# Performance work log

Hardware: AMD Instinct MI355X
Metric: run time of the kernel (lower is better)

Reference implementation:

```python
import jax, jax.numpy as jnp
import numpy as np

DT = 0.02
GRAVITY = jnp.array([0.0, -9.81, 0.0], dtype=jnp.float32)
RADIUS = 0.1125  # filter_extent/2 = 6*radius_scale*particle_radius/2
K3 = 4
TAPS = K3 ** 3
EPS = 1e-8
N_FLUID, N_BOX, KNBR = 8192, 4096, 48
BOX_L = 1.12
CORNERS = np.array([[dx, dy, dz] for dx in (0, 1) for dy in (0, 1) for dz in (0, 1)], np.int32)  # [8,3]


def _ball_to_cube(p):
    """Volume-preserving map unit-ball -> unit-cube (ball->cylinder->cube), per Open3D CConv."""
    x, y, z = p[..., 0], p[..., 1], p[..., 2]
    rxy2 = x * x + y * y
    rho = jnp.sqrt(rxy2 + z * z + EPS)
    rxy = jnp.sqrt(rxy2 + EPS)
    # ball -> cylinder
    pole = rxy2 <= 1.25 * z * z
    s_pole = jnp.sqrt(3.0 * rho / (rho + jnp.abs(z)))
    s_side = rho / rxy
    cx = jnp.where(pole, x * s_pole, x * s_side)
    cy = jnp.where(pole, y * s_pole, y * s_side)
    cz = jnp.where(pole, jnp.sign(z) * rho, 1.5 * z)
    # cylinder disc -> square (inverse concentric map)
    r = jnp.sqrt(cx * cx + cy * cy + EPS)
    cond = jnp.abs(cx) >= jnp.abs(cy)
    sx = jnp.where(cx >= 0, 1.0, -1.0)
    sy = jnp.where(cy >= 0, 1.0, -1.0)
    safe_cx = jnp.where(jnp.abs(cx) > EPS, cx, 1.0)
    safe_cy = jnp.where(jnp.abs(cy) > EPS, cy, 1.0)
    c4pi = 4.0 / jnp.pi
    u = jnp.where(cond, sx * r, sy * c4pi * r * jnp.arctan(cx / safe_cy))
    v = jnp.where(cond, sx * c4pi * r * jnp.arctan(cy / safe_cx), sy * r)
    tiny = rho < 1e-6
    return jnp.stack([jnp.where(tiny, 0.0, u), jnp.where(tiny, 0.0, v), jnp.where(tiny, 0.0, cz)], axis=-1)


def _cconv(feat_in, pos_in, pos_out, nbr_idx, filt, bias):
    """ContinuousConv: radius neighbors (padded, -1), poly6 window, trilinear interp over 4^3 taps."""
    Nq, K = nbr_idx.shape
    mask = (nbr_idx >= 0).astype(feat_in.dtype)
    idx = jnp.maximum(nbr_idx, 0)
    rel = (pos_in[idx] - pos_out[:, None, :]) / RADIUS            # [Nq,K,3]
    d2 = jnp.sum(rel * rel, axis=-1)
    win = jnp.clip((1.0 - d2) ** 3, 0.0, 1.0) * mask              # poly6 window on r^2
    cube = _ball_to_cube(rel)                                     # [-1,1]^3
    t = jnp.clip((cube * 0.5 + 0.5) * (K3 - 1), 0.0, K3 - 1.0)    # align_corners grid coords
    i0 = jnp.clip(jnp.floor(t), 0, K3 - 2).astype(jnp.int32)
    f = t - i0
    ci = i0[..., None, :] + CORNERS                               # [Nq,K,8,3]
    cw = jnp.prod(jnp.where(CORNERS[None, None] == 1, f[..., None, :], 1.0 - f[..., None, :]), axis=-1)
    tap = (ci[..., 0] * K3 + ci[..., 1]) * K3 + ci[..., 2]        # [Nq,K,8]
    cw = cw * win[..., None]
    ii = jnp.arange(Nq)[:, None, None]
    kk = jnp.arange(K)[None, :, None]
    Wt = jnp.zeros((Nq, K, TAPS), feat_in.dtype).at[ii, kk, tap].add(cw)  # [Nq,K,64]
    fnb = feat_in[idx]                                            # [Nq,K,Cin]
    A = jnp.einsum('nkt,nkc->ntc', Wt, fnb)                       # per-tap aggregated features
    return jnp.einsum('ntc,tcd->nd', A, filt.reshape(TAPS, filt.shape[-2], filt.shape[-1])) + bias


def _forward(pos, vel, box, box_feats, nbr_fluid, nbr_box, params):
    (cf0_w, cf0_b, co0_w, co0_b, d0_w, d0_b,
     c1_w, c1_b, d1_w, d1_b, c2_w, c2_b, d2_w, d2_b, c3_w, c3_b, d3_w, d3_b) = params
    vel_new = vel + GRAVITY * DT
    pos_new = pos + (vel + vel_new) * (0.5 * DT)
    fluid_feats = jnp.concatenate([jnp.ones_like(pos_new[:, :1]), vel_new], axis=-1)  # [N,4]
    a_conv = _cconv(fluid_feats, pos_new, pos_new, nbr_fluid, cf0_w, cf0_b)
    a_dense = fluid_feats @ d0_w + d0_b
    a_obs = _cconv(box_feats, box, pos_new, nbr_box, co0_w, co0_b)
    x = jnp.concatenate([a_obs, a_conv, a_dense], axis=-1)        # [N,96]
    for cw_, cb_, dw_, db_ in ((c1_w, c1_b, d1_w, d1_b), (c2_w, c2_b, d2_w, d2_b), (c3_w, c3_b, d3_w, d3_b)):
        h = jax.nn.relu(x)
        y = _cconv(h, pos_new, pos_new, nbr_fluid, cw_, cb_) + (h @ dw_ + db_)
        x = y + x if y.shape[-1] == x.shape[-1] else y            # dense residual when dims match
    pos_correction = x * (1.0 / 128.0)
    pos_new_corrected = pos_new + pos_correction
    vel_new_corrected = (pos_new_corrected - pos) / DT
    num_fluid_neighbors = jnp.sum((nbr_fluid >= 0).astype(jnp.float32), axis=-1)
    return pos_new_corrected, vel_new_corrected, num_fluid_neighbors


def _build_neighbors(queries, points, radius, K, exclude_self):
    N = queries.shape[0]
    idx = np.full((N, K), -1, np.int32)
    r2 = radius * radius
    chunk = 1024
    for s in range(0, N, chunk):
        q = queries[s:s + chunk]
        d2 = ((q[:, None, :] - points[None, :, :]) ** 2).sum(-1)
        within = d2 <= r2
        if exclude_self:
            rows = np.arange(q.shape[0])
            within[rows, s + rows] = False
        for r in range(q.shape[0]):
            nb = np.nonzero(within[r])[0][:K]
            idx[s + r, :nb.shape[0]] = nb
    return idx


def setup_inputs() -> dict:
    rng = np.random.default_rng(0)
    pos = rng.uniform(0.0, BOX_L, (N_FLUID, 3)).astype(np.float32)
    vel = (0.5 * rng.standard_normal((N_FLUID, 3))).astype(np.float32)
    box = rng.uniform(0.0, BOX_L, (N_BOX, 3)).astype(np.float32)
    box_feats = rng.standard_normal((N_BOX, 3)).astype(np.float32)
    g = np.array([0.0, -9.81, 0.0], np.float32)
    vel_new = vel + g * DT
    pos_new = pos + (vel + vel_new) * (0.5 * DT)
    nbr_fluid = _build_neighbors(pos_new, pos_new, RADIUS, KNBR, True)
    nbr_box = _build_neighbors(pos_new, box, RADIUS, KNBR, False)

    def xavier(*shape):
        fan_in = int(np.prod(shape[:-1]))
        lim = float(np.sqrt(6.0 / (fan_in + shape[-1])))
        return jnp.asarray(rng.uniform(-lim, lim, shape).astype(np.float32))

    z = lambda n: jnp.zeros((n,), jnp.float32)
    return {
        'pos': jnp.asarray(pos), 'vel': jnp.asarray(vel), 'box': jnp.asarray(box),
        'box_feats': jnp.asarray(box_feats),
        'nbr_fluid': jnp.asarray(nbr_fluid), 'nbr_box': jnp.asarray(nbr_box),
        'cf0_w': xavier(4, 4, 4, 4, 32), 'cf0_b': z(32),
        'co0_w': xavier(4, 4, 4, 3, 32), 'co0_b': z(32),
        'd0_w': xavier(4, 32), 'd0_b': z(32),
        'c1_w': xavier(4, 4, 4, 96, 64), 'c1_b': z(64), 'd1_w': xavier(96, 64), 'd1_b': z(64),
        'c2_w': xavier(4, 4, 4, 64, 64), 'c2_b': z(64), 'd2_w': xavier(64, 64), 'd2_b': z(64),
        'c3_w': xavier(4, 4, 4, 64, 3), 'c3_b': z(3), 'd3_w': xavier(64, 3), 'd3_b': z(3),
    }


def reference(pos, vel, box, box_feats, nbr_fluid, nbr_box,
              cf0_w, cf0_b, co0_w, co0_b, d0_w, d0_b,
              c1_w, c1_b, d1_w, d1_b, c2_w, c2_b, d2_w, d2_b, c3_w, c3_b, d3_w, d3_b):
    params = (cf0_w, cf0_b, co0_w, co0_b, d0_w, d0_b,
              c1_w, c1_b, d1_w, d1_b, c2_w, c2_b, d2_w, d2_b, c3_w, c3_b, d3_w, d3_b)
    return _forward(pos, vel, box, box_feats, nbr_fluid, nbr_box, params)
```

## Files before the change

kernel.cpp:

```cpp
#include <hip/hip_runtime.h>

#define NF 8192
#define KN 48
#define TM 8

typedef __attribute__((ext_vector_type(8))) short short8;
typedef __attribute__((ext_vector_type(4))) float f32x4;

__device__ __forceinline__ unsigned short bf16e(float f) {
    return (unsigned short)((__float_as_uint(f) + 0x8000u) >> 16);
}

__device__ __forceinline__ void pn_geom(float rx, float ry, float rz, unsigned* g)
{
    float d2  = rx * rx + ry * ry + rz * rz;
    float om  = 1.0f - d2;
    float win = om * om * om;
    win = fminf(fmaxf(win, 0.0f), 1.0f);

    float rxy2 = rx * rx + ry * ry;
    float rho  = sqrtf(rxy2 + rz * rz + 1e-8f);
    float rxyv = sqrtf(rxy2 + 1e-8f);
    bool  pole = (rxy2 <= 1.25f * rz * rz);
    float s    = pole ? sqrtf(3.0f * rho / (rho + fabsf(rz))) : (rho / rxyv);
    float cx = rx * s, cy = ry * s;
    float sgnz = (rz > 0.0f) ? 1.0f : ((rz < 0.0f) ? -1.0f : 0.0f);
    float cz   = pole ? sgnz * rho : 1.5f * rz;

    float rr   = sqrtf(cx * cx + cy * cy + 1e-8f);
    bool  cond = fabsf(cx) >= fabsf(cy);
    float sx = (cx >= 0.0f) ? 1.0f : -1.0f;
    float sy = (cy >= 0.0f) ? 1.0f : -1.0f;
    float safecx = (fabsf(cx) > 1e-8f) ? cx : 1.0f;
    float safecy = (fabsf(cy) > 1e-8f) ? cy : 1.0f;
    const float C4PI = 1.2732395447351628f;
    float u = cond ? (sx * rr) : (sy * C4PI * rr * atanf(cx / safecy));
    float v = cond ? (sx * C4PI * rr * atanf(cy / safecx)) : (sy * rr);
    if (rho < 1e-6f) { u = 0.0f; v = 0.0f; cz = 0.0f; }

    float tx = fminf(fmaxf((u  * 0.5f + 0.5f) * 3.0f, 0.0f), 3.0f);
    float ty = fminf(fmaxf((v  * 0.5f + 0.5f) * 3.0f, 0.0f), 3.0f);
    float tz = fminf(fmaxf((cz * 0.5f + 0.5f) * 3.0f, 0.0f), 3.0f);
    int ix = (int)floorf(tx); ix = ix < 0 ? 0 : (ix > 2 ? 2 : ix);
    int iy = (int)floorf(ty); iy = iy < 0 ? 0 : (iy > 2 ? 2 : iy);
    int iz = (int)floorf(tz); iz = iz < 0 ? 0 : (iz > 2 ? 2 : iz);
    float fx = tx - (float)ix, fy = ty - (float)iy, fz = tz - (float)iz;
    float wx0 = 1.0f - fx, wy0 = 1.0f - fy, wz0 = 1.0f - fz;

#pragma unroll
    for (int dx = 0; dx < 2; ++dx)
#pragma unroll
        for (int dy = 0; dy < 2; ++dy)
#pragma unroll
            for (int dz = 0; dz < 2; ++dz) {
                float w = (dx ? fx : wx0) * (dy ? fy : wy0) * (dz ? fz : wz0) * win;
                int tap = ((ix + dx) << 4) + ((iy + dy) << 2) + (iz + dz);
                g[(dx << 2) | (dy << 1) | dz] = ((unsigned)tap << 16) | (unsigned)bf16e(w);
            }
}

__global__ void __launch_bounds__(256) pn_prep(
    const float* __restrict__ pos, const float* __restrict__ vel,
    const int* __restrict__ nbrf,
    const float* __restrict__ d0w, const float* __restrict__ d0b,
    float* __restrict__ pos_new, float* __restrict__ feats0,
    float* __restrict__ X, float* __restrict__ nfn)
{
    int t = blockIdx.x * 256 + threadIdx.x;
    if (t >= NF) return;
    float vx = vel[t * 3 + 0], vy = vel[t * 3 + 1], vz = vel[t * 3 + 2];
    float vnx = vx, vny = vy - 9.81f * 0.02f, vnz = vz;
    float pnx = pos[t * 3 + 0] + (vx + vnx) * 0.01f;
    float pny = pos[t * 3 + 1] + (vy + vny) * 0.01f;
    float pnz = pos[t * 3 + 2] + (vz + vnz) * 0.01f;
    pos_new[t * 3 + 0] = pnx; pos_new[t * 3 + 1] = pny; pos_new[t * 3 + 2] = pnz;
    feats0[t * 4 + 0] = 1.0f; feats0[t * 4 + 1] = vnx;
    feats0[t * 4 + 2] = vny;  feats0[t * 4 + 3] = vnz;
    int cnt = 0;
    for (int k = 0; k < KN; ++k) cnt += (nbrf[t * KN + k] >= 0) ? 1 : 0;
    nfn[t] = (float)cnt;
    for (int j = 0; j < 32; ++j) {
        float s = d0b[j] + d0w[0 * 32 + j] + vnx * d0w[1 * 32 + j]
                + vny * d0w[2 * 32 + j] + vnz * d0w[3 * 32 + j];
        X[t * 96 + 64 + j] = s;
    }
}

template <int CIN, int COUT, int HAS_SELF>
__global__ void __launch_bounds__(256) pn_pack(
    const float* __restrict__ cw, const float* __restrict__ dw,
    const float* __restrict__ cb, const float* __restrict__ db,
    unsigned short* __restrict__ F2t, unsigned short* __restrict__ FD,
    float* __restrict__ B)
{
    constexpr int CINP = ((CIN + 15) / 16) * 16;
    constexpr int NCC  = CINP / 16;
    constexpr int DPAD = ((COUT + 15) / 16) * 16;
    constexpr int NT   = DPAD / 16;
    const int total1 = NCC * NT * 16 * 1024;
    const int total2 = HAS_SELF ? DPAD * CINP : 0;
    int i = blockIdx.x * 256 + threadIdx.x;
    if (i < total1) {
        int k2 = i & 1023;
        int q  = i >> 10;
        int dd = q & 15; q >>= 4;
        int dt = q % NT;
        int cc = q / NT;
        int t   = k2 >> 4;
        int cin = cc * 16 + (k2 & 15);
        int d   = dt * 16 + dd;
        float v = 0.0f;
        if (cin < CIN && d < COUT) v = cw[((size_t)t * CIN + cin) * COUT + d];
        F2t[i] = bf16e(v);
    } else if (i < total1 + total2) {
        int j = i - total1;
        int d = j / CINP, c = j % CINP;
        float v = 0.0f;
        if (c < CIN && d < COUT) v = dw[(size_t)c * COUT + d];
        FD[j] = bf16e(v);
    }
    if (i < COUT) B[i] = cb[i] + (HAS_SELF ? db[i] : 0.0f);
}

template <int CIN, int COUT, int HAS_SELF, int RELU_IN, int OUT_MODE>
__global__ void __launch_bounds__(512, 4) pn_cconv(
    const float* __restrict__ qpos, const float* __restrict__ ppos,
    const float* __restrict__ feats, const int* __restrict__ nbr,
    const unsigned short* __restrict__ F2t, const unsigned short* __restrict__ FD,
    const float* __restrict__ bias,
    const float* __restrict__ resid, float* __restrict__ outp,
    const float* __restrict__ pos0, int out_stride, int out_off)
{
    constexpr int CINP   = ((CIN + 15) / 16) * 16;
    constexpr int NCC    = CINP / 16;
    constexpr int DPAD   = ((COUT + 15) / 16) * 16;
    constexpr int NT     = DPAD / 16;
    constexpr int SPLITK = 8 / NT;
    constexpr int SPC2   = 32 / SPLITK;
    constexpr int WST    = 48;
    constexpr int A2ST   = 1032;

    __shared__ int      sI[TM * KN];
    __shared__ int      sKN[TM];
    __shared__ __align__(16) unsigned short sW [TM * 64 * WST];
    __shared__ __align__(16) unsigned short sFT[TM * 16 * WST];
    __shared__ __align__(16) unsigned short sA2[TM * A2ST];

    float*          sEpi = (float*)sFT;
    unsigned short* sA3  = sFT + 4096;

    const int tid  = threadIdx.x;
    const int w    = tid >> 6;
    const int lane = tid & 63;
    const int n16  = lane & 15;
    const int kg   = lane >> 4;
    const int pt0  = blockIdx.x * TM;
    const int dt   = w % NT;
    const int kh   = w / NT;

    if (tid < TM) sKN[tid] = KN;
    {
        uint4 z4 = make_uint4(0, 0, 0, 0);
        for (int i = tid; i < TM * 64 * WST / 8; i += 512) ((uint4*)sW)[i] = z4;
    }
    __syncthreads();

    for (int e = tid; e < TM * KN; e += 512) {
        int lp = e / KN, k = e - lp * KN;
        int q  = pt0 + lp;
        int id = nbr[q * KN + k];
        if (id >= 0) {
            sI[e] = id;
            float rx = (ppos[id * 3 + 0] - qpos[q * 3 + 0]) * (1.0f / 0.1125f);
            float ry = (ppos[id * 3 + 1] - qpos[q * 3 + 1]) * (1.0f / 0.1125f);
            float rz = (ppos[id * 3 + 2] - qpos[q * 3 + 2]) * (1.0f / 0.1125f);
            unsigned g[8];
            pn_geom(rx, ry, rz, g);
#pragma unroll
            for (int j = 0; j < 8; ++j)
                sW[(lp * 64 + (int)(g[j] >> 16)) * WST + k] = (unsigned short)(g[j] & 0xffffu);
        } else {
            atomicMin(&sKN[lp], k);
        }
    }

    f32x4 acc = {0.0f, 0.0f, 0.0f, 0.0f};
    __syncthreads();

    for (int cc = 0; cc < NCC; ++cc) {
        const int cb0 = cc * 16;

        for (int e = tid; e < TM * KN; e += 512) {
            int pt = e / KN, k = e - pt * KN;
            unsigned short vals[16];
            if (k < sKN[pt]) {
                int id = sI[e];
                if constexpr (CIN % 16 == 0) {
                    const float4* s4 = (const float4*)(feats + (size_t)id * CIN + cb0);
#pragma unroll
                    for (int v4 = 0; v4 < 4; ++v4) {
                        float4 f = s4[v4];
                        if (RELU_IN) { f.x=fmaxf(f.x,0.f); f.y=fmaxf(f.y,0.f); f.z=fmaxf(f.z,0.f); f.w=fmaxf(f.w,0.f); }
                        vals[v4*4+0] = bf16e(f.x); vals[v4*4+1] = bf16e(f.y);
                        vals[v4*4+2] = bf16e(f.z); vals[v4*4+3] = bf16e(f.w);
                    }
                } else {
#pragma unroll
                    for (int c = 0; c < 16; ++c) {
                        float f = (cb0 + c < CIN) ? feats[(size_t)id * CIN + cb0 + c] : 0.0f;
                        if (RELU_IN) f = fmaxf(f, 0.0f);
                        vals[c] = bf16e(f);
                    }
                }
            } else {
#pragma unroll
                for (int c = 0; c < 16; ++c) vals[c] = 0;
            }
#pragma unroll
            for (int c = 0; c < 16; ++c) sFT[(pt * 16 + c) * WST + k] = vals[c];
        }
        __syncthreads();

        {
            const short8 z8 = {0,0,0,0,0,0,0,0};
            short8 bv[2];
#pragma unroll
            for (int s = 0; s < 2; ++s) {
                int kidx = s * 32 + kg * 8;
                bv[s] = z8;
                if (kidx < KN)
                    bv[s] = *(const short8*)(sFT + (w * 16 + n16) * WST + kidx);
            }
#pragma unroll
            for (int mt = 0; mt < 4; ++mt) {
                f32x4 a1 = {0.0f, 0.0f, 0.0f, 0.0f};
#pragma unroll
                for (int s = 0; s < 2; ++s) {
                    int kidx = s * 32 + kg * 8;
                    short8 av = z8;
                    if (kidx < KN)
                        av = *(const short8*)(sW + (w * 64 + mt * 16 + n16) * WST + kidx);
                    a1 = __builtin_amdgcn_mfma_f32_16x16x32_bf16(av, bv[s], a1, 0, 0, 0);
                }
#pragma unroll
                for (int r = 0; r < 4; ++r)
                    sA2[w * A2ST + (mt * 16 + kg * 4 + r) * 16 + n16] = bf16e(a1[r]);
            }
        }
        __syncthreads();

        {
            const unsigned short* gB = F2t + ((size_t)((cc * NT + dt) * 16 + n16)) * 1024;
            const int s0 = kh * SPC2;
            const short8 z8 = {0,0,0,0,0,0,0,0};
#pragma unroll 4
            for (int s2 = 0; s2 < SPC2; ++s2) {
                int k2 = (s0 + s2) * 32 + kg * 8;
                short8 av = (n16 < TM) ? *(const short8*)(sA2 + n16 * A2ST + k2) : z8;
                short8 bv = *(const short8*)(gB + k2);
                acc = __builtin_amdgcn_mfma_f32_16x16x32_bf16(av, bv, acc, 0, 0, 0);
            }
        }
        __syncthreads();
    }

    if constexpr (HAS_SELF) {
        constexpr int NP = NCC / 2;
        for (int ccp = 0; ccp < NP; ++ccp) {
            if (tid < TM * 32) {
                int pt = tid / 32, c = tid & 31;
                int cin = ccp * 32 + c;
                float f = (cin < CIN) ? feats[(size_t)(pt0 + pt) * CIN + cin] : 0.0f;
                if (RELU_IN) f = fmaxf(f, 0.0f);
                sA3[pt * 40 + c] = bf16e(f);
            }
            __syncthreads();
            if (ccp % SPLITK == kh) {
                const short8 z8 = {0,0,0,0,0,0,0,0};
                short8 av = (n16 < TM) ? *(const short8*)(sA3 + n16 * 40 + kg * 8) : z8;
                short8 bv = *(const short8*)(FD + (size_t)(dt * 16 + n16) * CINP + ccp * 32 + kg * 8);
                acc = __builtin_amdgcn_mfma_f32_16x16x32_bf16(av, bv, acc, 0, 0, 0);
            }
            __syncthreads();
        }
    }

#pragma unroll
    for (int r = 0; r < 4; ++r) sEpi[(w * 64 + lane) * 4 + r] = acc[r];
    __syncthreads();

    if (w < NT) {
        float sum[4];
#pragma unroll
        for (int r = 0; r < 4; ++r) {
            float s = 0.0f;
#pragma unroll
            for (int k = 0; k < SPLITK; ++k)
                s += sEpi[((k * NT + w) * 64 + lane) * 4 + r];
            sum[r] = s;
        }
        int d = w * 16 + n16;
        if (d < COUT) {
            float b = bias[d];
#pragma unroll
            for (int r = 0; r < 4; ++r) {
                int pt = kg * 4 + r;
                if (pt < TM) {
                    int q = pt0 + pt;
                    float y = sum[r] + b;
                    if constexpr (OUT_MODE == 0) {
                        outp[q * out_stride + out_off + d] = y;
                    } else if constexpr (OUT_MODE == 1) {
                        outp[q * COUT + d] = y;
                    } else if constexpr (OUT_MODE == 2) {
                        outp[q * COUT + d] = y + resid[q * COUT + d];
                    } else {
                        float corr = y * (1.0f / 128.0f);
                        float pn   = qpos[q * 3 + d];
                        float pc   = pn + corr;
                        outp[q * 3 + d]          = pc;
                        outp[NF * 3 + q * 3 + d] = (pc - pos0[q * 3 + d]) * (1.0f / 0.02f);
                    }
                }
            }
        }
    }
}

extern "C" void kernel_launch(void* const* d_in, const int* in_sizes, int n_in,
                              void* d_out, int out_size, void* d_ws, size_t ws_size,
                              hipStream_t stream)
{
    (void)in_sizes; (void)n_in; (void)out_size; (void)ws_size;

    const float* pos       = (const float*)d_in[0];
    const float* vel       = (const float*)d_in[1];
    const float* box       = (const float*)d_in[2];
    const float* box_feats = (const float*)d_in[3];
    const int*   nbrf      = (const int*)d_in[4];
    const int*   nbrb      = (const int*)d_in[5];
    const float* cf0_w = (const float*)d_in[6];
    const float* cf0_b = (const float*)d_in[7];
    const float* co0_w = (const float*)d_in[8];
    const float* co0_b = (const float*)d_in[9];
    const float* d0_w  = (const float*)d_in[10];
    const float* d0_b  = (const float*)d_in[11];
    const float* c1_w  = (const float*)d_in[12];
    const float* c1_b  = (const float*)d_in[13];
    const float* d1_w  = (const float*)d_in[14];
    const float* d1_b  = (const float*)d_in[15];
    const float* c2_w  = (const float*)d_in[16];
    const float* c2_b  = (const float*)d_in[17];
    const float* d2_w  = (const float*)d_in[18];
    const float* d2_b  = (const float*)d_in[19];
    const float* c3_w  = (const float*)d_in[20];
    const float* c3_b  = (const float*)d_in[21];
    const float* d3_w  = (const float*)d_in[22];
    const float* d3_b  = (const float*)d_in[23];

    char* ws = (char*)d_ws;
    float*          POSNEW = (float*)(ws + 0);
    float*          FEATS0 = (float*)(ws + 98304);
    float*          X      = (float*)(ws + 229376);
    float*          X1     = (float*)(ws + 3375104);
    float*          X2     = (float*)(ws + 5472256);
    unsigned short* F2T1   = (unsigned short*)(ws + 7569408);
    unsigned short* F2T2   = (unsigned short*)(ws + 8355840);
    unsigned short* F2T3   = (unsigned short*)(ws + 8880128);
    unsigned short* F2Tf   = (unsigned short*)(ws + 9011200);
    unsigned short* F2To   = (unsigned short*)(ws + 9076736);
    unsigned short* FD1    = (unsigned short*)(ws + 9142272);
    unsigned short* FD2    = (unsigned short*)(ws + 9154560);
    unsigned short* FD3    = (unsigned short*)(ws + 9162752);
    float*          B1     = (float*)(ws + 9164800);
    float*          B2     = (float*)(ws + 9165056);
    float*          B3     = (float*)(ws + 9165312);
    float*          Bf0    = (float*)(ws + 9165568);
    float*          Bo0    = (float*)(ws + 9165824);

    float* out_f = (float*)d_out;

    pn_pack<96, 64, 1><<<(6*4*16*1024 + 64*96 + 255) / 256, 256, 0, stream>>>(c1_w, d1_w, c1_b, d1_b, F2T1, FD1, B1);
    pn_pack<64, 64, 1><<<(4*4*16*1024 + 64*64 + 255) / 256, 256, 0, stream>>>(c2_w, d2_w, c2_b, d2_b, F2T2, FD2, B2);
    pn_pack<64, 3, 1><<<(4*1*16*1024 + 16*64 + 255) / 256, 256, 0, stream>>>(c3_w, d3_w, c3_b, d3_b, F2T3, FD3, B3);
    pn_pack<4, 32, 0><<<(1*2*16*1024 + 255) / 256, 256, 0, stream>>>(cf0_w, nullptr, cf0_b, nullptr, F2Tf, nullptr, Bf0);
    pn_pack<3, 32, 0><<<(1*2*16*1024 + 255) / 256, 256, 0, stream>>>(co0_w, nullptr, co0_b, nullptr, F2To, nullptr, Bo0);

    pn_prep<<<(NF + 255) / 256, 256, 0, stream>>>(pos, vel, nbrf, d0_w, d0_b,
                                                  POSNEW, FEATS0, X, out_f + NF * 6);

    pn_cconv<4, 32, 0, 0, 0><<<NF / TM, 512, 0, stream>>>(
        POSNEW, POSNEW, FEATS0, nbrf, F2Tf, nullptr, Bf0, nullptr, X, nullptr, 96, 32);
    pn_cconv<3, 32, 0, 0, 0><<<NF / TM, 512, 0, stream>>>(
        POSNEW, box, box_feats, nbrb, F2To, nullptr, Bo0, nullptr, X, nullptr, 96, 0);
    pn_cconv<96, 64, 1, 1, 1><<<NF / TM, 512, 0, stream>>>(
        POSNEW, POSNEW, X, nbrf, F2T1, FD1, B1, nullptr, X1, nullptr, 0, 0);
    pn_cconv<64, 64, 1, 1, 2><<<NF / TM, 512, 0, stream>>>(
        POSNEW, POSNEW, X1, nbrf, F2T2, FD2, B2, X1, X2, nullptr, 0, 0);
    pn_cconv<64, 3, 1, 1, 3><<<NF / TM, 512, 0, stream>>>(
        POSNEW, POSNEW, X2, nbrf, F2T3, FD3, B3, nullptr, out_f, pos, 0, 0);
}
```

Before: 369.2 us.

## Halve tap-weight LDS via two tap-half passes and pipeline feature staging

Splits the 64-tap interpolation weights into two passes of 32 taps, halving the sW and sA2 shared buffers, and raises launch bounds so more blocks fit per CU. Neighbor geometry is now kept in registers, one thread per neighbor, which removes the sI/sKN arrays and the atomicMin. Staging of the next channel chunk is moved between the two MFMA stages to overlap global loads with compute, and two accumulators break the MFMA dependency chain. The cost is recomputing sW scatters and re-staging features for each half, plus extra register pressure under the tighter launch bound.

```diff
diff --git a/kernel.cpp b/kernel.cpp
--- a/kernel.cpp
+++ b/kernel.cpp
@@ -123,7 +123,7 @@
 }
 
 template <int CIN, int COUT, int HAS_SELF, int RELU_IN, int OUT_MODE>
-__global__ void __launch_bounds__(512, 4) pn_cconv(
+__global__ void __launch_bounds__(512, 6) pn_cconv(
     const float* __restrict__ qpos, const float* __restrict__ ppos,
     const float* __restrict__ feats, const int* __restrict__ nbr,
     const unsigned short* __restrict__ F2t, const unsigned short* __restrict__ FD,
@@ -136,13 +136,11 @@
     constexpr int DPAD   = ((COUT + 15) / 16) * 16;
     constexpr int NT     = DPAD / 16;
     constexpr int SPLITK = 8 / NT;
-    constexpr int SPC2   = 32 / SPLITK;
+    constexpr int SPC2H  = 16 / SPLITK;
     constexpr int WST    = 48;
-    constexpr int A2ST   = 1032;
-
-    __shared__ int      sI[TM * KN];
-    __shared__ int      sKN[TM];
-    __shared__ __align__(16) unsigned short sW [TM * 64 * WST];
+    constexpr int A2ST   = 520;
+
+    __shared__ __align__(16) unsigned short sW [TM * 32 * WST];
     __shared__ __align__(16) unsigned short sFT[TM * 16 * WST];
     __shared__ __align__(16) unsigned short sA2[TM * A2ST];
 
@@ -158,45 +156,28 @@
     const int dt   = w % NT;
     const int kh   = w / NT;
 
-    if (tid < TM) sKN[tid] = KN;
-    {
-        uint4 z4 = make_uint4(0, 0, 0, 0);
-        for (int i = tid; i < TM * 64 * WST / 8; i += 512) ((uint4*)sW)[i] = z4;
-    }
-    __syncthreads();
-
-    for (int e = tid; e < TM * KN; e += 512) {
-        int lp = e / KN, k = e - lp * KN;
-        int q  = pt0 + lp;
-        int id = nbr[q * KN + k];
-        if (id >= 0) {
-            sI[e] = id;
-            float rx = (ppos[id * 3 + 0] - qpos[q * 3 + 0]) * (1.0f / 0.1125f);
-            float ry = (ppos[id * 3 + 1] - qpos[q * 3 + 1]) * (1.0f / 0.1125f);
-            float rz = (ppos[id * 3 + 2] - qpos[q * 3 + 2]) * (1.0f / 0.1125f);
-            unsigned g[8];
+    const int myPt = tid / KN;
+    const int myK  = tid - myPt * KN;
+    int      myId  = -1;
+    unsigned g[8];
+    if (tid < TM * KN) {
+        int q = pt0 + myPt;
+        myId  = nbr[q * KN + myK];
+        if (myId >= 0) {
+            float rx = (ppos[myId * 3 + 0] - qpos[q * 3 + 0]) * (1.0f / 0.1125f);
+            float ry = (ppos[myId * 3 + 1] - qpos[q * 3 + 1]) * (1.0f / 0.1125f);
+            float rz = (ppos[myId * 3 + 2] - qpos[q * 3 + 2]) * (1.0f / 0.1125f);
             pn_geom(rx, ry, rz, g);
-#pragma unroll
-            for (int j = 0; j < 8; ++j)
-                sW[(lp * 64 + (int)(g[j] >> 16)) * WST + k] = (unsigned short)(g[j] & 0xffffu);
-        } else {
-            atomicMin(&sKN[lp], k);
-        }
-    }
-
-    f32x4 acc = {0.0f, 0.0f, 0.0f, 0.0f};
-    __syncthreads();
-
-    for (int cc = 0; cc < NCC; ++cc) {
-        const int cb0 = cc * 16;
-
-        for (int e = tid; e < TM * KN; e += 512) {
-            int pt = e / KN, k = e - pt * KN;
+        }
+    }
+
+    auto stage = [&](int cc) {
+        if (tid < TM * KN) {
+            const int cb0 = cc * 16;
             unsigned short vals[16];
-            if (k < sKN[pt]) {
-                int id = sI[e];
+            if (myId >= 0) {
                 if constexpr (CIN % 16 == 0) {
-                    const float4* s4 = (const float4*)(feats + (size_t)id * CIN + cb0);
+                    const float4* s4 = (const float4*)(feats + (size_t)myId * CIN + cb0);
 #pragma unroll
                     for (int v4 = 0; v4 < 4; ++v4) {
                         float4 f = s4[v4];
@@ -207,7 +188,7 @@
                 } else {
 #pragma unroll
                     for (int c = 0; c < 16; ++c) {
-                        float f = (cb0 + c < CIN) ? feats[(size_t)id * CIN + cb0 + c] : 0.0f;
+                        float f = (cb0 + c < CIN) ? feats[(size_t)myId * CIN + cb0 + c] : 0.0f;
                         if (RELU_IN) f = fmaxf(f, 0.0f);
                         vals[c] = bf16e(f);
                     }
@@ -217,51 +198,76 @@
                 for (int c = 0; c < 16; ++c) vals[c] = 0;
             }
 #pragma unroll
-            for (int c = 0; c < 16; ++c) sFT[(pt * 16 + c) * WST + k] = vals[c];
-        }
+            for (int c = 0; c < 16; ++c) sFT[(myPt * 16 + c) * WST + myK] = vals[c];
+        }
+    };
+
+    f32x4 accA = {0.0f, 0.0f, 0.0f, 0.0f};
+    f32x4 accB = {0.0f, 0.0f, 0.0f, 0.0f};
+    const short8 z8 = {0,0,0,0,0,0,0,0};
+
+    for (int th = 0; th < 2; ++th) {
         __syncthreads();
-
         {
-            const short8 z8 = {0,0,0,0,0,0,0,0};
-            short8 bv[2];
-#pragma unroll
-            for (int s = 0; s < 2; ++s) {
-                int kidx = s * 32 + kg * 8;
-                bv[s] = z8;
-                if (kidx < KN)
-                    bv[s] = *(const short8*)(sFT + (w * 16 + n16) * WST + kidx);
-            }
-#pragma unroll
-            for (int mt = 0; mt < 4; ++mt) {
-                f32x4 a1 = {0.0f, 0.0f, 0.0f, 0.0f};
+            uint4 z4 = make_uint4(0, 0, 0, 0);
+            for (int i = tid; i < TM * 32 * WST / 8; i += 512) ((uint4*)sW)[i] = z4;
+        }
+        __syncthreads();
+        if (tid < TM * KN && myId >= 0) {
+#pragma unroll
+            for (int j = 0; j < 8; ++j) {
+                unsigned tl = (g[j] >> 16) - (unsigned)(th * 32);
+                if (tl < 32u)
+                    sW[(myPt * 32 + (int)tl) * WST + myK] = (unsigned short)(g[j] & 0xffffu);
+            }
+        }
+        stage(0);
+        __syncthreads();
+
+        for (int cc = 0; cc < NCC; ++cc) {
+            {
+                short8 bvv[2];
 #pragma unroll
                 for (int s = 0; s < 2; ++s) {
                     int kidx = s * 32 + kg * 8;
-                    short8 av = z8;
+                    bvv[s] = z8;
                     if (kidx < KN)
-                        av = *(const short8*)(sW + (w * 64 + mt * 16 + n16) * WST + kidx);
-                    a1 = __builtin_amdgcn_mfma_f32_16x16x32_bf16(av, bv[s], a1, 0, 0, 0);
+                        bvv[s] = *(const short8*)(sFT + (w * 16 + n16) * WST + kidx);
                 }
 #pragma unroll
-                for (int r = 0; r < 4; ++r)
-                    sA2[w * A2ST + (mt * 16 + kg * 4 + r) * 16 + n16] = bf16e(a1[r]);
-            }
-        }
-        __syncthreads();
-
-        {
-            const unsigned short* gB = F2t + ((size_t)((cc * NT + dt) * 16 + n16)) * 1024;
-            const int s0 = kh * SPC2;
-            const short8 z8 = {0,0,0,0,0,0,0,0};
-#pragma unroll 4
-            for (int s2 = 0; s2 < SPC2; ++s2) {
-                int k2 = (s0 + s2) * 32 + kg * 8;
-                short8 av = (n16 < TM) ? *(const short8*)(sA2 + n16 * A2ST + k2) : z8;
-                short8 bv = *(const short8*)(gB + k2);
-                acc = __builtin_amdgcn_mfma_f32_16x16x32_bf16(av, bv, acc, 0, 0, 0);
-            }
-        }
-        __syncthreads();
+                for (int ml = 0; ml < 2; ++ml) {
+                    f32x4 a1 = {0.0f, 0.0f, 0.0f, 0.0f};
+#pragma unroll
+                    for (int s = 0; s < 2; ++s) {
+                        int kidx = s * 32 + kg * 8;
+                        short8 av = z8;
+                        if (kidx < KN)
+                            av = *(const short8*)(sW + (w * 32 + ml * 16 + n16) * WST + kidx);
+                        a1 = __builtin_amdgcn_mfma_f32_16x16x32_bf16(av, bvv[s], a1, 0, 0, 0);
+                    }
+#pragma unroll
+                    for (int r = 0; r < 4; ++r)
+                        sA2[w * A2ST + (ml * 16 + kg * 4 + r) * 16 + n16] = bf16e(a1[r]);
+                }
+            }
+            __syncthreads();
+
+            if (cc + 1 < NCC) stage(cc + 1);
+
+            {
+                const unsigned short* gB =
+                    F2t + ((size_t)((cc * NT + dt) * 16 + n16)) * 1024 + th * 512;
+#pragma unroll
+                for (int s2 = 0; s2 < SPC2H; ++s2) {
+                    int k2l = (kh * SPC2H + s2) * 32 + kg * 8;
+                    short8 av = (n16 < TM) ? *(const short8*)(sA2 + n16 * A2ST + k2l) : z8;
+                    short8 bv = *(const short8*)(gB + k2l);
+                    if (s2 & 1) accB = __builtin_amdgcn_mfma_f32_16x16x32_bf16(av, bv, accB, 0, 0, 0);
+                    else        accA = __builtin_amdgcn_mfma_f32_16x16x32_bf16(av, bv, accA, 0, 0, 0);
+                }
+            }
+            __syncthreads();
+        }
     }
 
     if constexpr (HAS_SELF) {
@@ -276,17 +282,16 @@
             }
             __syncthreads();
             if (ccp % SPLITK == kh) {
-                const short8 z8 = {0,0,0,0,0,0,0,0};
                 short8 av = (n16 < TM) ? *(const short8*)(sA3 + n16 * 40 + kg * 8) : z8;
                 short8 bv = *(const short8*)(FD + (size_t)(dt * 16 + n16) * CINP + ccp * 32 + kg * 8);
-                acc = __builtin_amdgcn_mfma_f32_16x16x32_bf16(av, bv, acc, 0, 0, 0);
+                accA = __builtin_amdgcn_mfma_f32_16x16x32_bf16(av, bv, accA, 0, 0, 0);
             }
             __syncthreads();
         }
     }
 
 #pragma unroll
-    for (int r = 0; r < 4; ++r) sEpi[(w * 64 + lane) * 4 + r] = acc[r];
+    for (int r = 0; r < 4; ++r) sEpi[(w * 64 + lane) * 4 + r] = accA[r] + accB[r];
     __syncthreads();
 
     if (w < NT) {
```

New measurement: 443.9 us. 1.2x slower.
